# Performance work log

Measured on AMD Instinct MI355X. Metric: run time of the kernel, lower is better.

The kernel has to match this reference:

```python
import jax, jax.numpy as jnp
import numpy as np

GAMMA = 1.0
BIG = 1e10  # finite stand-in for +inf boundary; exp(-BIG) underflows to exactly 0 (grad-safe)


def setup_inputs() -> dict:
    key = jax.random.key(0)
    k1, k2 = jax.random.split(key)
    B, L, C = 64, 1024, 64
    x = jax.random.normal(k1, (B, L, C), dtype=jnp.float32)
    y = jax.random.normal(k2, (B, L, C), dtype=jnp.float32)
    return {"x": x, "y": y}


def _soft_dtw(x, y, gamma=GAMMA):
    B, L, C = x.shape
    # squared-euclidean pairwise cost, scaled by 1/gamma (matches torch code)
    x2 = jnp.sum(x * x, axis=-1)[:, :, None]            # [B,L,1]
    y2 = jnp.sum(y * y, axis=-1)[:, None, :]            # [B,1,L]
    D = (x2 + y2 - 2.0 * jnp.einsum('blc,bmc->blm', x, y)) / gamma  # [B,L,L]

    # Anti-diagonal wavefront DP over the (L+2)x(L+2) R matrix.
    # r_d[i] holds R[i, d-i] for the diagonal i+j=d, i in 0..L+1.
    n = L + 2
    ii = jnp.arange(n)
    i_idx = jnp.clip(ii - 1, 0, L - 1)
    r_prev2 = jnp.full((B, n), BIG, dtype=x.dtype).at[:, 0].set(0.0)  # diag d=0: R[0,0]=0
    r_prev1 = jnp.full((B, n), BIG, dtype=x.dtype)                    # diag d=1: all boundary
    big_col = jnp.full((B, 1), BIG, dtype=x.dtype)

    def step(carry, d):
        rp2, rp1 = carry
        jj = d - ii
        valid = (ii >= 1) & (ii <= L) & (jj >= 1) & (jj <= L)
        j_idx = jnp.clip(jj - 1, 0, L - 1)
        d_vals = D[:, i_idx, j_idx]                                   # [B,n] cost along diagonal
        r_diag = jnp.concatenate([big_col, rp2[:, :-1]], axis=1)      # R[i-1, j-1]
        r_up   = jnp.concatenate([big_col, rp1[:, :-1]], axis=1)      # R[i-1, j]
        r_left = rp1                                                  # R[i,   j-1]
        z = jnp.stack([-r_diag, -r_up, -r_left], axis=-1)             # [B,n,3]
        zmax = jnp.max(z, axis=-1)
        softmin = -(jnp.log(jnp.sum(jnp.exp(z - zmax[..., None]), axis=-1)) + zmax)
        new = jnp.where(valid[None, :], d_vals + softmin, BIG)
        return (rp1, new), None

    (_, r_last), _ = jax.lax.scan(step, (r_prev2, r_prev1), jnp.arange(2, 2 * L + 1))
    # last diagonal is d=2L; R[L,L] sits at index i=L
    return r_last[:, L] * gamma


def reference(x, y):
    return _soft_dtw(x, y)
```

## Files before the change

kernel.cpp:

```cpp
#include <hip/hip_runtime.h>


typedef unsigned short ushort_t;
typedef __attribute__((ext_vector_type(8))) short short8;
typedef __attribute__((ext_vector_type(4))) float f32x4;
typedef __attribute__((ext_vector_type(4))) unsigned short ushort4v;

constexpr int B_ = 64, L_ = 1024, C_ = 64;
constexpr int DSTR = 130;
constexpr int HBSTR = 1280;

#define BIGV 1e10f
#define INV_LN2 1.44269504088896340736f
#define LN2F 0.69314718055994530942f
#define DPP_WAVE_SHL1 0x130
#define DPP_WAVE_SHR1 0x138

static __device__ __forceinline__ ushort_t f2bf(float f) {
  unsigned u = __builtin_bit_cast(unsigned, f);
  unsigned r = (u + 0x7fffu + ((u >> 16) & 1u)) >> 16;
  return (ushort_t)r;
}
static __device__ __forceinline__ float exp2_(float x) {
  float r; asm("v_exp_f32 %0, %1" : "=v"(r) : "v"(x)); return r;
}
static __device__ __forceinline__ float log2_(float x) {
  float r; asm("v_log_f32 %0, %1" : "=v"(r) : "v"(x)); return r;
}
static __device__ __forceinline__ unsigned cvt_pk_bf16(float lo, float hi) {
  unsigned r; asm("v_cvt_pk_bf16_f32 %0, %1, %2" : "=v"(r) : "v"(lo), "v"(hi)); return r;
}
static __device__ __forceinline__ float dpp_shr1(float old, float src) {
  return __builtin_bit_cast(float, __builtin_amdgcn_update_dpp(
      __builtin_bit_cast(int, old), __builtin_bit_cast(int, src),
      DPP_WAVE_SHR1, 0xF, 0xF, false));
}
static __device__ __forceinline__ float dpp_shl1(float v) {
  return __builtin_bit_cast(float, __builtin_amdgcn_update_dpp(
      __builtin_bit_cast(int, v), __builtin_bit_cast(int, v),
      DPP_WAVE_SHL1, 0xF, 0xF, false));
}

__global__ __launch_bounds__(256) void prep_kernel(
    const float* __restrict__ x, const float* __restrict__ y,
    ushort_t* __restrict__ xb, ushort_t* __restrict__ yb,
    float* __restrict__ x2, float* __restrict__ y2, int* __restrict__ flagsG)
{
  if (blockIdx.x == 0 && threadIdx.x < 192) flagsG[threadIdx.x] = 0;
  const int lane = threadIdx.x & 63;
  const int sub = lane >> 4;
  const int cg  = lane & 15;
  const int wv = (blockIdx.x * blockDim.x + threadIdx.x) >> 6;
  const int nw = (gridDim.x * blockDim.x) >> 6;
  const int totalGroups = (2 * B_ * L_) >> 2;
  for (int g = wv; g < totalGroups; g += nw) {
    int r = g * 4 + sub;
    const float* src; ushort_t* dst; float* nrm;
    if (r < B_ * L_) { src = x; dst = xb; nrm = x2; }
    else             { r -= B_ * L_; src = y; dst = yb; nrm = y2; }
    const float4 v = *(const float4*)(src + (size_t)r * C_ + cg * 4);
    ushort4v p;
    p.x = f2bf(v.x); p.y = f2bf(v.y); p.z = f2bf(v.z); p.w = f2bf(v.w);
    *(ushort4v*)(dst + (size_t)r * C_ + cg * 4) = p;
    float s = v.x*v.x + v.y*v.y + v.z*v.z + v.w*v.w;
    s += __shfl_xor(s, 1); s += __shfl_xor(s, 2);
    s += __shfl_xor(s, 4); s += __shfl_xor(s, 8);
    if (cg == 0) nrm[r] = s * INV_LN2;
  }
}

template<int HDST, bool FIRST>
static __device__ __forceinline__ void dp_chunk(
    const int t, const int lane, float& cur, float& dgp, float hvv,
    const float zsel, const ushort_t* __restrict__ DtwLane,
    float* __restrict__ HbDst, float* __restrict__ HXB)
{
  const unsigned* pw = (const unsigned*)(DtwLane + ((t << 6) & 127));
  const int cb = (t << 6) - 63;
  unsigned a0 = pw[0], a1 = pw[1], b0 = pw[2], b1 = pw[3];

  auto step = [&](unsigned dw, int k, int u) -> float {
    float dv = __builtin_bit_cast(float, (k & 1) ? (dw & 0xffff0000u) : (dw << 16));
    float up = dpp_shr1(hvv, cur);
    float dg = dgp, lf = cur;
    if constexpr (FIRST) {
      bool at0 = (u == lane);
      dg = at0 ? zsel : dg;
      lf = at0 ? BIGV : lf;
    }
    float mn = fminf(fminf(up, dg), lf);
    float e = exp2_(mn - up) + exp2_(mn - dg) + exp2_(mn - lf);
    float nv = (dv + mn) - log2_(e);
    dgp = up;
    hvv = dpp_shl1(hvv);
    if constexpr (FIRST) { if (u >= lane) cur = nv; }
    else cur = nv;
    return nv;
  };
  auto flush4 = [&](int c0, float v0, float v1, float v2, float v3) {
    if constexpr (HDST == 0) {
      if (lane == 63) { HbDst[c0] = v0; HbDst[c0+1] = v1; HbDst[c0+2] = v2; HbDst[c0+3] = v3; }
    } else if constexpr (HDST == 1) {
      if (lane == 63) { HXB[c0] = v0; HXB[c0+1] = v1; HXB[c0+2] = v2; HXB[c0+3] = v3; }
    }
  };

  #pragma unroll 1
  for (int g = 0; g < 8; ++g) {
    const int u0 = g * 8;
    unsigned n0 = 0, n1 = 0, n2 = 0, n3 = 0;
    if (g < 7) {
      n0 = pw[u0/2 + 4]; n1 = pw[u0/2 + 5]; n2 = pw[u0/2 + 6]; n3 = pw[u0/2 + 7];
    }
    float v0 = step(a0, 0, u0 + 0);
    float v1 = step(a0, 1, u0 + 1);
    float v2 = step(a1, 0, u0 + 2);
    float v3 = step(a1, 1, u0 + 3);
    if constexpr (!FIRST) flush4(cb + u0, v0, v1, v2, v3);
    float v4 = step(b0, 0, u0 + 4);
    float v5 = step(b0, 1, u0 + 5);
    float v6 = step(b1, 0, u0 + 6);
    float v7 = step(b1, 1, u0 + 7);
    if constexpr (!FIRST) flush4(cb + u0 + 4, v4, v5, v6, v7);
    a0 = n0; a1 = n1; b0 = n2; b1 = n3;
    (void)v0; (void)v1; (void)v2; (void)v3; (void)v4; (void)v5; (void)v6; (void)v7;
  }
  if constexpr (FIRST) {
    if constexpr (HDST == 0) { if (lane == 63) HbDst[0] = cur; }
    else if constexpr (HDST == 1) { if (lane == 63) HXB[0] = cur; }
  }
}

template<int HDST>
static __device__ __forceinline__ void dp_tail(
    const int lane, float& cur, float& dgp,
    const ushort_t* __restrict__ DtwLane,
    float* __restrict__ HbDst, float* __restrict__ HXB)
{
  const unsigned* pw = (const unsigned*)(DtwLane);
  #pragma unroll 1
  for (int g = 0; g < 8; ++g) {
    unsigned w0 = pw[g*4], w1 = pw[g*4+1], w2 = pw[g*4+2], w3 = pw[g*4+3];
    #pragma unroll
    for (int k = 0; k < 8; ++k) {
      const int u = g * 8 + k;
      unsigned dw = (k < 2) ? w0 : (k < 4) ? w1 : (k < 6) ? w2 : w3;
      float dv = __builtin_bit_cast(float, (k & 1) ? (dw & 0xffff0000u) : (dw << 16));
      float up = dpp_shr1(BIGV, cur);
      float dg = dgp, lf = cur;
      float mn = fminf(fminf(up, dg), lf);
      float e = exp2_(mn - up) + exp2_(mn - dg) + exp2_(mn - lf);
      float nv = (dv + mn) - log2_(e);
      dgp = up;
      if (u < lane) {
        cur = nv;
        if constexpr (HDST == 0) { if (lane == 63) HbDst[961 + u] = nv; }
        else if constexpr (HDST == 1) { if (lane == 63) HXB[961 + u] = nv; }
      }
    }
  }
}

static __device__ __forceinline__ void spin_lds(int* f, int v) {
  int k = 0;
  while (__hip_atomic_load(f, __ATOMIC_ACQUIRE, __HIP_MEMORY_SCOPE_WORKGROUP) < v) {
    __builtin_amdgcn_s_sleep(1);
    if (++k > (1 << 26)) break;
  }
}
static __device__ __forceinline__ void spin_glb(int* f, int v) {
  int k = 0;
  while (__hip_atomic_load(f, __ATOMIC_ACQUIRE, __HIP_MEMORY_SCOPE_AGENT) < v) {
    __builtin_amdgcn_s_sleep(8);
    if (++k > (1 << 26)) break;
  }
}

template<int HSRC, int HDST>
static __device__ __forceinline__ void run_band(
    const ushort_t* __restrict__ xbB, const ushort_t* __restrict__ ybB,
    const float* __restrict__ x2B, const float* __restrict__ y2B,
    const float* __restrict__ HXin, float* __restrict__ HXout,
    int* __restrict__ fGin, int* __restrict__ fGout,
    ushort_t* __restrict__ Dtw, const float* __restrict__ HbSrc,
    float* __restrict__ HbDst, int* __restrict__ cin, int* __restrict__ cout,
    const int lane, const int W, float* __restrict__ outp)
{
  const int m = lane & 15, q = lane >> 4;
  const int i0 = W * 64;

  short8 af[4][2];
  #pragma unroll
  for (int mt = 0; mt < 4; ++mt)
    #pragma unroll
    for (int ks = 0; ks < 2; ++ks)
      af[mt][ks] = *(const short8*)(xbB + (size_t)(i0 + mt * 16 + m) * C_ + ks * 32 + q * 8);
  f32x4 x2q[4];
  #pragma unroll
  for (int mt = 0; mt < 4; ++mt) x2q[mt] = *(const f32x4*)(x2B + i0 + mt * 16 + q * 4);

  short8 bfr0[4], bfr1[4];
  auto load_bfr = [&](int tc) {
    const ushort_t* yb0 = ybB + (size_t)tc * 64 * C_;
    #pragma unroll
    for (int nt = 0; nt < 4; ++nt) {
      bfr0[nt] = *(const short8*)(yb0 + (size_t)(nt * 16 + m) * C_ + q * 8);
      bfr1[nt] = *(const short8*)(yb0 + (size_t)(nt * 16 + m) * C_ + 32 + q * 8);
    }
  };
  auto gram = [&](int tc) {
    const int cb = tc * 64;
    const float* y2j = y2B + cb;
    #pragma unroll
    for (int mt = 0; mt < 4; ++mt) {
      const int r0 = mt * 16 + q * 4;
      #pragma unroll
      for (int nt = 0; nt < 4; ++nt) {
        f32x4 acc = {0.f, 0.f, 0.f, 0.f};
        acc = __builtin_amdgcn_mfma_f32_16x16x32_bf16(af[mt][0], bfr0[nt], acc, 0, 0, 0);
        acc = __builtin_amdgcn_mfma_f32_16x16x32_bf16(af[mt][1], bfr1[nt], acc, 0, 0, 0);
        float y2v = y2j[nt * 16 + m];
        float d0 = fmaf(acc[0], -2.f * INV_LN2, x2q[mt][0] + y2v);
        float d1 = fmaf(acc[1], -2.f * INV_LN2, x2q[mt][1] + y2v);
        float d2 = fmaf(acc[2], -2.f * INV_LN2, x2q[mt][2] + y2v);
        float d3 = fmaf(acc[3], -2.f * INV_LN2, x2q[mt][3] + y2v);
        unsigned p01 = cvt_pk_bf16(d0, d1);
        unsigned p23 = cvt_pk_bf16(d2, d3);
        const int cs = cb + nt * 16 + m + r0;
        ushort_t* base = Dtw + r0 * DSTR;
        base[             ( cs      & 127)] = (ushort_t)p01;
        base[    DSTR  +  ((cs + 1) & 127)] = (ushort_t)(p01 >> 16);
        base[2 * DSTR  +  ((cs + 2) & 127)] = (ushort_t)p23;
        base[3 * DSTR  +  ((cs + 3) & 127)] = (ushort_t)(p23 >> 16);
      }
    }
  };

  float cur = 0.f, dgp = BIGV;
  const float zsel = (W == 0 && lane == 0) ? 0.f : BIGV;
  const ushort_t* DtwLane = Dtw + lane * DSTR;

  load_bfr(0);
  gram(0);

  #pragma unroll 1
  for (int t = 0; t < 16; ++t) {
    if (t < 15) load_bfr(t + 1);
    float hvv;
    if constexpr (HSRC == 0) {
      hvv = BIGV;
    } else if constexpr (HSRC == 1) {
      spin_lds(cin, t + 1);
      hvv = HbSrc[(t << 6) + lane];
    } else {
      spin_glb(fGin, t + 1);
      hvv = HXin[(t << 6) + lane];
    }
    if (t == 0) dp_chunk<HDST, true >(0, lane, cur, dgp, hvv, zsel, DtwLane, HbDst, HXout);
    else        dp_chunk<HDST, false>(t, lane, cur, dgp, hvv, zsel, DtwLane, HbDst, HXout);
    if constexpr (HDST == 0) {
      if (lane == 0) __hip_atomic_store(cout, t, __ATOMIC_RELEASE, __HIP_MEMORY_SCOPE_WORKGROUP);
    } else if constexpr (HDST == 1) {
      if (lane == 0) __hip_atomic_store(fGout, t, __ATOMIC_RELEASE, __HIP_MEMORY_SCOPE_AGENT);
    }
    if (t < 15) gram(t + 1);
  }
  dp_tail<HDST>(lane, cur, dgp, DtwLane, HbDst, HXout);
  if constexpr (HDST == 0) {
    if (lane == 0) __hip_atomic_store(cout, 16, __ATOMIC_RELEASE, __HIP_MEMORY_SCOPE_WORKGROUP);
  } else if constexpr (HDST == 1) {
    if (lane == 0) __hip_atomic_store(fGout, 16, __ATOMIC_RELEASE, __HIP_MEMORY_SCOPE_AGENT);
  }
  if (W == 15 && lane == 63) *outp = cur * LN2F;
}

__global__ __launch_bounds__(256) void sdtw_kernel(
    const ushort_t* __restrict__ xb, const ushort_t* __restrict__ yb,
    const float* __restrict__ x2g, const float* __restrict__ y2g,
    float* __restrict__ HXg, int* __restrict__ flagsG,
    float* __restrict__ out)
{
  __shared__ ushort_t Dt[4][64 * DSTR];
  __shared__ float Hb[3][HBSTR];
  __shared__ int cflag[4];

  const int b = blockIdx.x & 63;
  const int sub = blockIdx.x >> 6;
  const int w = threadIdx.x >> 6;
  const int lane = threadIdx.x & 63;
  const int W = sub * 4 + w;

  if (threadIdx.x < 4) cflag[threadIdx.x] = 0;
  __syncthreads();

  const ushort_t* xbB = xb + (size_t)b * L_ * C_;
  const ushort_t* ybB = yb + (size_t)b * L_ * C_;
  const float* x2B = x2g + b * L_;
  const float* y2B = y2g + b * L_;
  const float* HXin = HXg + ((size_t)b * 3 + (sub - 1)) * L_;
  float* HXout      = HXg + ((size_t)b * 3 + sub) * L_;
  int* fGin  = flagsG + b * 3 + (sub - 1);
  int* fGout = flagsG + b * 3 + sub;
  ushort_t* Dtw = &Dt[w][0];
  const float* HbSrc = (w > 0) ? &Hb[w - 1][0] : &Hb[0][0];
  float* HbDst = (w < 3) ? &Hb[w][0] : &Hb[0][0];
  int* cin  = (w > 0) ? &cflag[w - 1] : &cflag[0];
  int* cout = (w < 3) ? &cflag[w] : &cflag[3];
  float* outp = out + b;

  if (sub == 0) {
    if (w == 0)      run_band<0, 0>(xbB, ybB, x2B, y2B, HXin, HXout, fGin, fGout, Dtw, HbSrc, HbDst, cin, cout, lane, W, outp);
    else if (w < 3)  run_band<1, 0>(xbB, ybB, x2B, y2B, HXin, HXout, fGin, fGout, Dtw, HbSrc, HbDst, cin, cout, lane, W, outp);
    else             run_band<1, 1>(xbB, ybB, x2B, y2B, HXin, HXout, fGin, fGout, Dtw, HbSrc, HbDst, cin, cout, lane, W, outp);
  } else if (sub < 3) {
    if (w == 0)      run_band<2, 0>(xbB, ybB, x2B, y2B, HXin, HXout, fGin, fGout, Dtw, HbSrc, HbDst, cin, cout, lane, W, outp);
    else if (w < 3)  run_band<1, 0>(xbB, ybB, x2B, y2B, HXin, HXout, fGin, fGout, Dtw, HbSrc, HbDst, cin, cout, lane, W, outp);
    else             run_band<1, 1>(xbB, ybB, x2B, y2B, HXin, HXout, fGin, fGout, Dtw, HbSrc, HbDst, cin, cout, lane, W, outp);
  } else {
    if (w == 0)      run_band<2, 0>(xbB, ybB, x2B, y2B, HXin, HXout, fGin, fGout, Dtw, HbSrc, HbDst, cin, cout, lane, W, outp);
    else if (w < 3)  run_band<1, 0>(xbB, ybB, x2B, y2B, HXin, HXout, fGin, fGout, Dtw, HbSrc, HbDst, cin, cout, lane, W, outp);
    else             run_band<1, 2>(xbB, ybB, x2B, y2B, HXin, HXout, fGin, fGout, Dtw, HbSrc, HbDst, cin, cout, lane, W, outp);
  }
}

extern "C" void kernel_launch(void* const* d_in, const int* in_sizes, int n_in,
                              void* d_out, int out_size, void* d_ws, size_t ws_size,
                              hipStream_t stream) {
  const float* x = (const float*)d_in[0];
  const float* y = (const float*)d_in[1];
  float* out = (float*)d_out;

  char* ws = (char*)d_ws;
  const size_t XB = (size_t)B_ * L_ * C_ * 2;
  const size_t NB = (size_t)B_ * L_ * 4;
  ushort_t* xb = (ushort_t*)ws;
  ushort_t* yb = (ushort_t*)(ws + XB);
  float* x2 = (float*)(ws + 2 * XB);
  float* y2 = (float*)(ws + 2 * XB + NB);
  float* HX = (float*)(ws + 2 * XB + 2 * NB);
  int* flagsG = (int*)(ws + 2 * XB + 2 * NB + (size_t)B_ * 3 * L_ * 4);

  prep_kernel<<<512, 256, 0, stream>>>(x, y, xb, yb, x2, y2, flagsG);
  sdtw_kernel<<<256, 256, 0, stream>>>(xb, yb, x2, y2, HX, flagsG, out);
}
```

Before: 355.3 us.

## Replace log-sum-exp DP with scaled linear-domain recurrence using mantissa/exponent pairs

The soft-min recurrence moves out of log space. Each R cell is stored as a mantissa plus an integer base-2 exponent, so a step needs three ldexp scalings, a sum and a multiply by a precomputed exp2 of the fractional cost, instead of three exps and a log. The gram stage now precomputes, per cell, the integer part of the cost and an fp16 exp2 of its fractional part, packed into 32-bit LDS words. Halo buffers double in size to carry (mantissa, exponent) pairs, and the global spin sleep is shortened. The fp16 cost factor and integer flooring change numerics relative to the fp32 log-space reference.

```diff
diff --git a/kernel.cpp b/kernel.cpp
--- a/kernel.cpp
+++ b/kernel.cpp
@@ -7,38 +7,33 @@
 typedef __attribute__((ext_vector_type(4))) unsigned short ushort4v;
 
 constexpr int B_ = 64, L_ = 1024, C_ = 64;
-constexpr int DSTR = 130;
-constexpr int HBSTR = 1280;
-
-#define BIGV 1e10f
+constexpr int DSTRW = 129;
+
+#define BIGS (-(1 << 24))
 #define INV_LN2 1.44269504088896340736f
 #define LN2F 0.69314718055994530942f
-#define DPP_WAVE_SHL1 0x130
-#define DPP_WAVE_SHR1 0x138
 
 static __device__ __forceinline__ ushort_t f2bf(float f) {
   unsigned u = __builtin_bit_cast(unsigned, f);
   unsigned r = (u + 0x7fffu + ((u >> 16) & 1u)) >> 16;
   return (ushort_t)r;
 }
-static __device__ __forceinline__ float exp2_(float x) {
-  float r; asm("v_exp_f32 %0, %1" : "=v"(r) : "v"(x)); return r;
-}
-static __device__ __forceinline__ float log2_(float x) {
-  float r; asm("v_log_f32 %0, %1" : "=v"(r) : "v"(x)); return r;
-}
-static __device__ __forceinline__ unsigned cvt_pk_bf16(float lo, float hi) {
-  unsigned r; asm("v_cvt_pk_bf16_f32 %0, %1, %2" : "=v"(r) : "v"(lo), "v"(hi)); return r;
-}
 static __device__ __forceinline__ float dpp_shr1(float old, float src) {
   return __builtin_bit_cast(float, __builtin_amdgcn_update_dpp(
-      __builtin_bit_cast(int, old), __builtin_bit_cast(int, src),
-      DPP_WAVE_SHR1, 0xF, 0xF, false));
+      __builtin_bit_cast(int, old), __builtin_bit_cast(int, src), 0x138, 0xF, 0xF, false));
+}
+static __device__ __forceinline__ int dpp_shr1_i(int old, int src) {
+  return __builtin_amdgcn_update_dpp(old, src, 0x138, 0xF, 0xF, false);
 }
 static __device__ __forceinline__ float dpp_shl1(float v) {
   return __builtin_bit_cast(float, __builtin_amdgcn_update_dpp(
-      __builtin_bit_cast(int, v), __builtin_bit_cast(int, v),
-      DPP_WAVE_SHL1, 0xF, 0xF, false));
+      __builtin_bit_cast(int, v), __builtin_bit_cast(int, v), 0x130, 0xF, 0xF, false));
+}
+static __device__ __forceinline__ int dpp_shl1_i(int v) {
+  return __builtin_amdgcn_update_dpp(v, v, 0x130, 0xF, 0xF, false);
+}
+static __device__ __forceinline__ int imax3(int a, int b, int c) {
+  int m = a > b ? a : b; return c > m ? c : m;
 }
 
 __global__ __launch_bounds__(256) void prep_kernel(
@@ -65,97 +60,113 @@
     float s = v.x*v.x + v.y*v.y + v.z*v.z + v.w*v.w;
     s += __shfl_xor(s, 1); s += __shfl_xor(s, 2);
     s += __shfl_xor(s, 4); s += __shfl_xor(s, 8);
-    if (cg == 0) nrm[r] = s * INV_LN2;
+    if (cg == 0) nrm[r] = s * INV_LN2 + 0.25f;
   }
 }
 
 template<int HDST, bool FIRST>
 static __device__ __forceinline__ void dp_chunk(
-    const int t, const int lane, float& cur, float& dgp, float hvv,
-    const float zsel, const ushort_t* __restrict__ DtwLane,
-    float* __restrict__ HbDst, float* __restrict__ HXB)
-{
-  const unsigned* pw = (const unsigned*)(DtwLane + ((t << 6) & 127));
+    const int t, const int lane,
+    float& cur_u, int& cur_S, float& dgp_u, int& dgp_S,
+    float hv_u, int hv_S, const float zu, const int zS,
+    const unsigned* __restrict__ DtLane,
+    float2* __restrict__ HbDst, float2* __restrict__ HXB)
+{
+  const unsigned* pw = DtLane + ((t & 1) << 6);
   const int cb = (t << 6) - 63;
-  unsigned a0 = pw[0], a1 = pw[1], b0 = pw[2], b1 = pw[3];
-
-  auto step = [&](unsigned dw, int k, int u) -> float {
-    float dv = __builtin_bit_cast(float, (k & 1) ? (dw & 0xffff0000u) : (dw << 16));
-    float up = dpp_shr1(hvv, cur);
-    float dg = dgp, lf = cur;
+  unsigned d0=pw[0],d1=pw[1],d2=pw[2],d3=pw[3],d4=pw[4],d5=pw[5],d6=pw[6],d7=pw[7];
+
+  auto step = [&](unsigned dw, int u) {
+    float up_u = dpp_shr1(hv_u, cur_u);
+    int   up_S = dpp_shr1_i(hv_S, cur_S);
+    hv_u = dpp_shl1(hv_u);
+    hv_S = dpp_shl1_i(hv_S);
+    float p = (float)__builtin_bit_cast(_Float16, (unsigned short)(dw & 0xffffu));
+    int di = (int)(dw >> 16);
+    float dg_u = dgp_u, lf_u = cur_u;
+    int   dg_S = dgp_S, lf_S = cur_S;
     if constexpr (FIRST) {
-      bool at0 = (u == lane);
-      dg = at0 ? zsel : dg;
-      lf = at0 ? BIGV : lf;
-    }
-    float mn = fminf(fminf(up, dg), lf);
-    float e = exp2_(mn - up) + exp2_(mn - dg) + exp2_(mn - lf);
-    float nv = (dv + mn) - log2_(e);
-    dgp = up;
-    hvv = dpp_shl1(hvv);
-    if constexpr (FIRST) { if (u >= lane) cur = nv; }
-    else cur = nv;
-    return nv;
-  };
-  auto flush4 = [&](int c0, float v0, float v1, float v2, float v3) {
-    if constexpr (HDST == 0) {
-      if (lane == 63) { HbDst[c0] = v0; HbDst[c0+1] = v1; HbDst[c0+2] = v2; HbDst[c0+3] = v3; }
-    } else if constexpr (HDST == 1) {
-      if (lane == 63) { HXB[c0] = v0; HXB[c0+1] = v1; HXB[c0+2] = v2; HXB[c0+3] = v3; }
+      const bool a0 = (u == lane);
+      dg_u = a0 ? zu : dg_u;  dg_S = a0 ? zS : dg_S;
+      lf_u = a0 ? 0.f : lf_u; lf_S = a0 ? BIGS : lf_S;
+    }
+    int Sm = imax3(up_S, dg_S, lf_S);
+    float sa = ldexpf(up_u, up_S - Sm);
+    float sb = ldexpf(dg_u, dg_S - Sm);
+    float sc = ldexpf(lf_u, lf_S - Sm);
+    float un = ((sa + sb) + sc) * p;
+    int ub = __float_as_int(un);
+    int ex = ((ub >> 23) & 0xff) - 126;
+    float mant = __int_as_float((ub & 0x007fffff) | 0x3f000000);
+    int Sn = Sm - di + ex;
+    dgp_u = up_u; dgp_S = up_S;
+    const bool wr = FIRST ? (u >= lane) : true;
+    if (wr) { cur_u = mant; cur_S = Sn; }
+    if constexpr (!FIRST && HDST != 2) {
+      if (lane == 63) {
+        float2 pr; pr.x = mant; pr.y = __int_as_float(Sn);
+        if constexpr (HDST == 0) HbDst[cb + u] = pr;
+        else                     HXB[cb + u] = pr;
+      }
     }
   };
 
   #pragma unroll 1
   for (int g = 0; g < 8; ++g) {
-    const int u0 = g * 8;
-    unsigned n0 = 0, n1 = 0, n2 = 0, n3 = 0;
+    unsigned n0=0,n1=0,n2=0,n3=0,n4=0,n5=0,n6=0,n7=0;
     if (g < 7) {
-      n0 = pw[u0/2 + 4]; n1 = pw[u0/2 + 5]; n2 = pw[u0/2 + 6]; n3 = pw[u0/2 + 7];
-    }
-    float v0 = step(a0, 0, u0 + 0);
-    float v1 = step(a0, 1, u0 + 1);
-    float v2 = step(a1, 0, u0 + 2);
-    float v3 = step(a1, 1, u0 + 3);
-    if constexpr (!FIRST) flush4(cb + u0, v0, v1, v2, v3);
-    float v4 = step(b0, 0, u0 + 4);
-    float v5 = step(b0, 1, u0 + 5);
-    float v6 = step(b1, 0, u0 + 6);
-    float v7 = step(b1, 1, u0 + 7);
-    if constexpr (!FIRST) flush4(cb + u0 + 4, v4, v5, v6, v7);
-    a0 = n0; a1 = n1; b0 = n2; b1 = n3;
-    (void)v0; (void)v1; (void)v2; (void)v3; (void)v4; (void)v5; (void)v6; (void)v7;
-  }
-  if constexpr (FIRST) {
-    if constexpr (HDST == 0) { if (lane == 63) HbDst[0] = cur; }
-    else if constexpr (HDST == 1) { if (lane == 63) HXB[0] = cur; }
+      const unsigned* np = pw + ((g + 1) << 3);
+      n0=np[0]; n1=np[1]; n2=np[2]; n3=np[3]; n4=np[4]; n5=np[5]; n6=np[6]; n7=np[7];
+    }
+    const int u0 = g << 3;
+    step(d0, u0+0); step(d1, u0+1); step(d2, u0+2); step(d3, u0+3);
+    step(d4, u0+4); step(d5, u0+5); step(d6, u0+6); step(d7, u0+7);
+    d0=n0; d1=n1; d2=n2; d3=n3; d4=n4; d5=n5; d6=n6; d7=n7;
+  }
+  if constexpr (FIRST && HDST != 2) {
+    if (lane == 63) {
+      float2 pr; pr.x = cur_u; pr.y = __int_as_float(cur_S);
+      if constexpr (HDST == 0) HbDst[0] = pr; else HXB[0] = pr;
+    }
   }
 }
 
 template<int HDST>
 static __device__ __forceinline__ void dp_tail(
-    const int lane, float& cur, float& dgp,
-    const ushort_t* __restrict__ DtwLane,
-    float* __restrict__ HbDst, float* __restrict__ HXB)
-{
-  const unsigned* pw = (const unsigned*)(DtwLane);
+    const int lane, float& cur_u, int& cur_S, float& dgp_u, int& dgp_S,
+    const unsigned* __restrict__ DtLane,
+    float2* __restrict__ HbDst, float2* __restrict__ HXB)
+{
+  const unsigned* pw = DtLane;
   #pragma unroll 1
   for (int g = 0; g < 8; ++g) {
-    unsigned w0 = pw[g*4], w1 = pw[g*4+1], w2 = pw[g*4+2], w3 = pw[g*4+3];
+    unsigned w0=pw[g*8],w1=pw[g*8+1],w2=pw[g*8+2],w3=pw[g*8+3],
+             w4=pw[g*8+4],w5=pw[g*8+5],w6=pw[g*8+6],w7=pw[g*8+7];
     #pragma unroll
     for (int k = 0; k < 8; ++k) {
       const int u = g * 8 + k;
-      unsigned dw = (k < 2) ? w0 : (k < 4) ? w1 : (k < 6) ? w2 : w3;
-      float dv = __builtin_bit_cast(float, (k & 1) ? (dw & 0xffff0000u) : (dw << 16));
-      float up = dpp_shr1(BIGV, cur);
-      float dg = dgp, lf = cur;
-      float mn = fminf(fminf(up, dg), lf);
-      float e = exp2_(mn - up) + exp2_(mn - dg) + exp2_(mn - lf);
-      float nv = (dv + mn) - log2_(e);
-      dgp = up;
+      unsigned dw = (k==0)?w0:(k==1)?w1:(k==2)?w2:(k==3)?w3:(k==4)?w4:(k==5)?w5:(k==6)?w6:w7;
+      float up_u = dpp_shr1(0.f, cur_u);
+      int   up_S = dpp_shr1_i(BIGS, cur_S);
+      float p = (float)__builtin_bit_cast(_Float16, (unsigned short)(dw & 0xffffu));
+      int di = (int)(dw >> 16);
+      int Sm = imax3(up_S, dgp_S, cur_S);
+      float sa = ldexpf(up_u, up_S - Sm);
+      float sb = ldexpf(dgp_u, dgp_S - Sm);
+      float sc = ldexpf(cur_u, cur_S - Sm);
+      float un = ((sa + sb) + sc) * p;
+      int ub = __float_as_int(un);
+      int ex = ((ub >> 23) & 0xff) - 126;
+      float mant = __int_as_float((ub & 0x007fffff) | 0x3f000000);
+      int Sn = Sm - di + ex;
+      dgp_u = up_u; dgp_S = up_S;
       if (u < lane) {
-        cur = nv;
-        if constexpr (HDST == 0) { if (lane == 63) HbDst[961 + u] = nv; }
-        else if constexpr (HDST == 1) { if (lane == 63) HXB[961 + u] = nv; }
+        cur_u = mant; cur_S = Sn;
+        if (lane == 63) {
+          float2 pr; pr.x = mant; pr.y = __int_as_float(Sn);
+          if constexpr (HDST == 0) HbDst[961 + u] = pr;
+          else if constexpr (HDST == 1) HXB[961 + u] = pr;
+        }
       }
     }
   }
@@ -171,7 +182,7 @@
 static __device__ __forceinline__ void spin_glb(int* f, int v) {
   int k = 0;
   while (__hip_atomic_load(f, __ATOMIC_ACQUIRE, __HIP_MEMORY_SCOPE_AGENT) < v) {
-    __builtin_amdgcn_s_sleep(8);
+    __builtin_amdgcn_s_sleep(2);
     if (++k > (1 << 26)) break;
   }
 }
@@ -180,10 +191,10 @@
 static __device__ __forceinline__ void run_band(
     const ushort_t* __restrict__ xbB, const ushort_t* __restrict__ ybB,
     const float* __restrict__ x2B, const float* __restrict__ y2B,
-    const float* __restrict__ HXin, float* __restrict__ HXout,
+    const float2* __restrict__ HXin, float2* __restrict__ HXout,
     int* __restrict__ fGin, int* __restrict__ fGout,
-    ushort_t* __restrict__ Dtw, const float* __restrict__ HbSrc,
-    float* __restrict__ HbDst, int* __restrict__ cin, int* __restrict__ cout,
+    unsigned* __restrict__ Dtw, const float2* __restrict__ HbSrc,
+    float2* __restrict__ HbDst, int* __restrict__ cin, int* __restrict__ cout,
     const int lane, const int W, float* __restrict__ outp)
 {
   const int m = lane & 15, q = lane >> 4;
@@ -200,17 +211,18 @@
   for (int mt = 0; mt < 4; ++mt) x2q[mt] = *(const f32x4*)(x2B + i0 + mt * 16 + q * 4);
 
   short8 bfr0[4], bfr1[4];
+  f32x4 y2r = {0.f, 0.f, 0.f, 0.f};
   auto load_bfr = [&](int tc) {
     const ushort_t* yb0 = ybB + (size_t)tc * 64 * C_;
     #pragma unroll
     for (int nt = 0; nt < 4; ++nt) {
       bfr0[nt] = *(const short8*)(yb0 + (size_t)(nt * 16 + m) * C_ + q * 8);
       bfr1[nt] = *(const short8*)(yb0 + (size_t)(nt * 16 + m) * C_ + 32 + q * 8);
+      y2r[nt] = y2B[tc * 64 + nt * 16 + m];
     }
   };
   auto gram = [&](int tc) {
     const int cb = tc * 64;
-    const float* y2j = y2B + cb;
     #pragma unroll
     for (int mt = 0; mt < 4; ++mt) {
       const int r0 = mt * 16 + q * 4;
@@ -219,26 +231,34 @@
         f32x4 acc = {0.f, 0.f, 0.f, 0.f};
         acc = __builtin_amdgcn_mfma_f32_16x16x32_bf16(af[mt][0], bfr0[nt], acc, 0, 0, 0);
         acc = __builtin_amdgcn_mfma_f32_16x16x32_bf16(af[mt][1], bfr1[nt], acc, 0, 0, 0);
-        float y2v = y2j[nt * 16 + m];
-        float d0 = fmaf(acc[0], -2.f * INV_LN2, x2q[mt][0] + y2v);
-        float d1 = fmaf(acc[1], -2.f * INV_LN2, x2q[mt][1] + y2v);
-        float d2 = fmaf(acc[2], -2.f * INV_LN2, x2q[mt][2] + y2v);
-        float d3 = fmaf(acc[3], -2.f * INV_LN2, x2q[mt][3] + y2v);
-        unsigned p01 = cvt_pk_bf16(d0, d1);
-        unsigned p23 = cvt_pk_bf16(d2, d3);
+        const float y2v = y2r[nt];
         const int cs = cb + nt * 16 + m + r0;
-        ushort_t* base = Dtw + r0 * DSTR;
-        base[             ( cs      & 127)] = (ushort_t)p01;
-        base[    DSTR  +  ((cs + 1) & 127)] = (ushort_t)(p01 >> 16);
-        base[2 * DSTR  +  ((cs + 2) & 127)] = (ushort_t)p23;
-        base[3 * DSTR  +  ((cs + 3) & 127)] = (ushort_t)(p23 >> 16);
+        #pragma unroll
+        for (int reg = 0; reg < 4; ++reg) {
+          float d = fmaf(acc[reg], -2.f * INV_LN2, x2q[mt][reg] + y2v);
+          d = fmaxf(d, 0.5f);
+          int di = (int)d;
+          float pe = (float)di + 0.5f - d;
+          float p = __builtin_amdgcn_exp2f(pe);
+          unsigned short hb = __builtin_bit_cast(unsigned short, (_Float16)p);
+          Dtw[(r0 + reg) * DSTRW + ((cs + reg) & 127)] = ((unsigned)di << 16) | (unsigned)hb;
+        }
       }
     }
   };
-
-  float cur = 0.f, dgp = BIGV;
-  const float zsel = (W == 0 && lane == 0) ? 0.f : BIGV;
-  const ushort_t* DtwLane = Dtw + lane * DSTR;
+  auto signal = [&](int v) {
+    if constexpr (HDST == 0) {
+      if (lane == 0) __hip_atomic_store(cout, v, __ATOMIC_RELEASE, __HIP_MEMORY_SCOPE_WORKGROUP);
+    } else if constexpr (HDST == 1) {
+      if (lane == 0) __hip_atomic_store(fGout, v, __ATOMIC_RELEASE, __HIP_MEMORY_SCOPE_AGENT);
+    }
+  };
+
+  float cur_u = 0.f, dgp_u = 0.f;
+  int cur_S = BIGS, dgp_S = BIGS;
+  const float zu = (W == 0 && lane == 0) ? 1.0f : 0.f;
+  const int   zS = (W == 0 && lane == 0) ? 0 : BIGS;
+  const unsigned* DtLane = Dtw + lane * DSTRW;
 
   load_bfr(0);
   gram(0);
@@ -246,42 +266,41 @@
   #pragma unroll 1
   for (int t = 0; t < 16; ++t) {
     if (t < 15) load_bfr(t + 1);
-    float hvv;
+    float hv_u; int hv_S;
     if constexpr (HSRC == 0) {
-      hvv = BIGV;
+      hv_u = 0.f; hv_S = BIGS;
     } else if constexpr (HSRC == 1) {
       spin_lds(cin, t + 1);
-      hvv = HbSrc[(t << 6) + lane];
+      float2 pr = HbSrc[(t << 6) + lane];
+      hv_u = pr.x; hv_S = __float_as_int(pr.y);
     } else {
       spin_glb(fGin, t + 1);
-      hvv = HXin[(t << 6) + lane];
-    }
-    if (t == 0) dp_chunk<HDST, true >(0, lane, cur, dgp, hvv, zsel, DtwLane, HbDst, HXout);
-    else        dp_chunk<HDST, false>(t, lane, cur, dgp, hvv, zsel, DtwLane, HbDst, HXout);
-    if constexpr (HDST == 0) {
-      if (lane == 0) __hip_atomic_store(cout, t, __ATOMIC_RELEASE, __HIP_MEMORY_SCOPE_WORKGROUP);
-    } else if constexpr (HDST == 1) {
-      if (lane == 0) __hip_atomic_store(fGout, t, __ATOMIC_RELEASE, __HIP_MEMORY_SCOPE_AGENT);
-    }
+      float2 pr = HXin[(t << 6) + lane];
+      hv_u = pr.x; hv_S = __float_as_int(pr.y);
+    }
+    if (t == 0)
+      dp_chunk<HDST, true >(0, lane, cur_u, cur_S, dgp_u, dgp_S, hv_u, hv_S, zu, zS, DtLane, HbDst, HXout);
+    else
+      dp_chunk<HDST, false>(t, lane, cur_u, cur_S, dgp_u, dgp_S, hv_u, hv_S, zu, zS, DtLane, HbDst, HXout);
+    signal(t);
     if (t < 15) gram(t + 1);
   }
-  dp_tail<HDST>(lane, cur, dgp, DtwLane, HbDst, HXout);
-  if constexpr (HDST == 0) {
-    if (lane == 0) __hip_atomic_store(cout, 16, __ATOMIC_RELEASE, __HIP_MEMORY_SCOPE_WORKGROUP);
-  } else if constexpr (HDST == 1) {
-    if (lane == 0) __hip_atomic_store(fGout, 16, __ATOMIC_RELEASE, __HIP_MEMORY_SCOPE_AGENT);
-  }
-  if (W == 15 && lane == 63) *outp = cur * LN2F;
+  dp_tail<HDST>(lane, cur_u, cur_S, dgp_u, dgp_S, DtLane, HbDst, HXout);
+  signal(16);
+  if (W == 15 && lane == 63) {
+    float uu = fmaxf(cur_u, 1e-30f);
+    *outp = (-(float)cur_S - __builtin_amdgcn_logf(uu)) * LN2F;
+  }
 }
 
 __global__ __launch_bounds__(256) void sdtw_kernel(
     const ushort_t* __restrict__ xb, const ushort_t* __restrict__ yb,
     const float* __restrict__ x2g, const float* __restrict__ y2g,
-    float* __restrict__ HXg, int* __restrict__ flagsG,
+    float2* __restrict__ HXg, int* __restrict__ flagsG,
     float* __restrict__ out)
 {
-  __shared__ ushort_t Dt[4][64 * DSTR];
-  __shared__ float Hb[3][HBSTR];
+  __shared__ unsigned Dt[4][64 * DSTRW];
+  __shared__ float2 Hb[3][1024];
   __shared__ int cflag[4];
 
   const int b = blockIdx.x & 63;
@@ -297,13 +316,13 @@
   const ushort_t* ybB = yb + (size_t)b * L_ * C_;
   const float* x2B = x2g + b * L_;
   const float* y2B = y2g + b * L_;
-  const float* HXin = HXg + ((size_t)b * 3 + (sub - 1)) * L_;
-  float* HXout      = HXg + ((size_t)b * 3 + sub) * L_;
-  int* fGin  = flagsG + b * 3 + (sub - 1);
-  int* fGout = flagsG + b * 3 + sub;
-  ushort_t* Dtw = &Dt[w][0];
-  const float* HbSrc = (w > 0) ? &Hb[w - 1][0] : &Hb[0][0];
-  float* HbDst = (w < 3) ? &Hb[w][0] : &Hb[0][0];
+  const float2* HXin = HXg + ((size_t)b * 3 + (sub > 0 ? sub - 1 : 0)) * L_;
+  float2* HXout      = HXg + ((size_t)b * 3 + (sub < 3 ? sub : 2)) * L_;
+  int* fGin  = flagsG + b * 3 + (sub > 0 ? sub - 1 : 0);
+  int* fGout = flagsG + b * 3 + (sub < 3 ? sub : 2);
+  unsigned* Dtw = &Dt[w][0];
+  const float2* HbSrc = (w > 0) ? &Hb[w - 1][0] : &Hb[0][0];
+  float2* HbDst = (w < 3) ? &Hb[w][0] : &Hb[0][0];
   int* cin  = (w > 0) ? &cflag[w - 1] : &cflag[0];
   int* cout = (w < 3) ? &cflag[w] : &cflag[3];
   float* outp = out + b;
@@ -337,8 +356,8 @@
   ushort_t* yb = (ushort_t*)(ws + XB);
   float* x2 = (float*)(ws + 2 * XB);
   float* y2 = (float*)(ws + 2 * XB + NB);
-  float* HX = (float*)(ws + 2 * XB + 2 * NB);
-  int* flagsG = (int*)(ws + 2 * XB + 2 * NB + (size_t)B_ * 3 * L_ * 4);
+  float2* HX = (float2*)(ws + 2 * XB + 2 * NB);
+  int* flagsG = (int*)(ws + 2 * XB + 2 * NB + (size_t)B_ * 3 * L_ * 8);
 
   prep_kernel<<<512, 256, 0, stream>>>(x, y, xb, yb, x2, y2, flagsG);
   sdtw_kernel<<<256, 256, 0, stream>>>(xb, yb, x2, y2, HX, flagsG, out);
```

After: 469.5 us. +32.1%, slower.

## Use 8-wave blocks with two blocks per batch and a cheaper softmin

Applied to the files above, without the earlier changes.

Each batch element is now handled by 2 blocks of 8 waves (512 threads) instead of 4 blocks of 4 waves. That replaces two of the three cross-block global-flag handoffs with in-LDS handoffs between waves. The softmin is rewritten to sort the three inputs so that one exp2 becomes the constant 1, leaving two exp2 plus a log. The global spin sleep is also shortened. The larger block needs more LDS and registers per workgroup, which may limit residency.

```diff
diff --git a/kernel.cpp b/kernel.cpp
--- a/kernel.cpp
+++ b/kernel.cpp
@@ -8,37 +8,26 @@
 
 constexpr int B_ = 64, L_ = 1024, C_ = 64;
 constexpr int DSTR = 130;
-constexpr int HBSTR = 1280;
 
 #define BIGV 1e10f
 #define INV_LN2 1.44269504088896340736f
 #define LN2F 0.69314718055994530942f
-#define DPP_WAVE_SHL1 0x130
-#define DPP_WAVE_SHR1 0x138
 
 static __device__ __forceinline__ ushort_t f2bf(float f) {
   unsigned u = __builtin_bit_cast(unsigned, f);
   unsigned r = (u + 0x7fffu + ((u >> 16) & 1u)) >> 16;
   return (ushort_t)r;
 }
-static __device__ __forceinline__ float exp2_(float x) {
-  float r; asm("v_exp_f32 %0, %1" : "=v"(r) : "v"(x)); return r;
-}
-static __device__ __forceinline__ float log2_(float x) {
-  float r; asm("v_log_f32 %0, %1" : "=v"(r) : "v"(x)); return r;
-}
 static __device__ __forceinline__ unsigned cvt_pk_bf16(float lo, float hi) {
   unsigned r; asm("v_cvt_pk_bf16_f32 %0, %1, %2" : "=v"(r) : "v"(lo), "v"(hi)); return r;
 }
 static __device__ __forceinline__ float dpp_shr1(float old, float src) {
   return __builtin_bit_cast(float, __builtin_amdgcn_update_dpp(
-      __builtin_bit_cast(int, old), __builtin_bit_cast(int, src),
-      DPP_WAVE_SHR1, 0xF, 0xF, false));
+      __builtin_bit_cast(int, old), __builtin_bit_cast(int, src), 0x138, 0xF, 0xF, false));
 }
 static __device__ __forceinline__ float dpp_shl1(float v) {
   return __builtin_bit_cast(float, __builtin_amdgcn_update_dpp(
-      __builtin_bit_cast(int, v), __builtin_bit_cast(int, v),
-      DPP_WAVE_SHL1, 0xF, 0xF, false));
+      __builtin_bit_cast(int, v), __builtin_bit_cast(int, v), 0x130, 0xF, 0xF, false));
 }
 
 __global__ __launch_bounds__(256) void prep_kernel(
@@ -46,7 +35,7 @@
     ushort_t* __restrict__ xb, ushort_t* __restrict__ yb,
     float* __restrict__ x2, float* __restrict__ y2, int* __restrict__ flagsG)
 {
-  if (blockIdx.x == 0 && threadIdx.x < 192) flagsG[threadIdx.x] = 0;
+  if (blockIdx.x == 0 && threadIdx.x < 64) flagsG[threadIdx.x] = 0;
   const int lane = threadIdx.x & 63;
   const int sub = lane >> 4;
   const int cg  = lane & 15;
@@ -72,10 +61,10 @@
 template<int HDST, bool FIRST>
 static __device__ __forceinline__ void dp_chunk(
     const int t, const int lane, float& cur, float& dgp, float hvv,
-    const float zsel, const ushort_t* __restrict__ DtwLane,
+    const float zsel, const ushort_t* __restrict__ DtLane,
     float* __restrict__ HbDst, float* __restrict__ HXB)
 {
-  const unsigned* pw = (const unsigned*)(DtwLane + ((t << 6) & 127));
+  const unsigned* pw = (const unsigned*)(DtLane + ((t << 6) & 127));
   const int cb = (t << 6) - 63;
   unsigned a0 = pw[0], a1 = pw[1], b0 = pw[2], b1 = pw[3];
 
@@ -89,8 +78,10 @@
       lf = at0 ? BIGV : lf;
     }
     float mn = fminf(fminf(up, dg), lf);
-    float e = exp2_(mn - up) + exp2_(mn - dg) + exp2_(mn - lf);
-    float nv = (dv + mn) - log2_(e);
+    float mx = fmaxf(fmaxf(up, dg), lf);
+    float md = fmaxf(fminf(up, dg), fminf(fmaxf(up, dg), lf));
+    float e = 1.0f + (__builtin_amdgcn_exp2f(mn - md) + __builtin_amdgcn_exp2f(mn - mx));
+    float nv = (dv + mn) - __builtin_amdgcn_logf(e);
     dgp = up;
     hvv = dpp_shl1(hvv);
     if constexpr (FIRST) { if (u >= lane) cur = nv; }
@@ -134,10 +125,10 @@
 template<int HDST>
 static __device__ __forceinline__ void dp_tail(
     const int lane, float& cur, float& dgp,
-    const ushort_t* __restrict__ DtwLane,
+    const ushort_t* __restrict__ DtLane,
     float* __restrict__ HbDst, float* __restrict__ HXB)
 {
-  const unsigned* pw = (const unsigned*)(DtwLane);
+  const unsigned* pw = (const unsigned*)(DtLane);
   #pragma unroll 1
   for (int g = 0; g < 8; ++g) {
     unsigned w0 = pw[g*4], w1 = pw[g*4+1], w2 = pw[g*4+2], w3 = pw[g*4+3];
@@ -149,13 +140,17 @@
       float up = dpp_shr1(BIGV, cur);
       float dg = dgp, lf = cur;
       float mn = fminf(fminf(up, dg), lf);
-      float e = exp2_(mn - up) + exp2_(mn - dg) + exp2_(mn - lf);
-      float nv = (dv + mn) - log2_(e);
+      float mx = fmaxf(fmaxf(up, dg), lf);
+      float md = fmaxf(fminf(up, dg), fminf(fmaxf(up, dg), lf));
+      float e = 1.0f + (__builtin_amdgcn_exp2f(mn - md) + __builtin_amdgcn_exp2f(mn - mx));
+      float nv = (dv + mn) - __builtin_amdgcn_logf(e);
       dgp = up;
       if (u < lane) {
         cur = nv;
-        if constexpr (HDST == 0) { if (lane == 63) HbDst[961 + u] = nv; }
-        else if constexpr (HDST == 1) { if (lane == 63) HXB[961 + u] = nv; }
+        if (lane == 63) {
+          if constexpr (HDST == 0) HbDst[961 + u] = nv;
+          else if constexpr (HDST == 1) HXB[961 + u] = nv;
+        }
       }
     }
   }
@@ -171,7 +166,7 @@
 static __device__ __forceinline__ void spin_glb(int* f, int v) {
   int k = 0;
   while (__hip_atomic_load(f, __ATOMIC_ACQUIRE, __HIP_MEMORY_SCOPE_AGENT) < v) {
-    __builtin_amdgcn_s_sleep(8);
+    __builtin_amdgcn_s_sleep(2);
     if (++k > (1 << 26)) break;
   }
 }
@@ -235,10 +230,17 @@
       }
     }
   };
+  auto signal = [&](int v) {
+    if constexpr (HDST == 0) {
+      if (lane == 0) __hip_atomic_store(cout, v, __ATOMIC_RELEASE, __HIP_MEMORY_SCOPE_WORKGROUP);
+    } else if constexpr (HDST == 1) {
+      if (lane == 0) __hip_atomic_store(fGout, v, __ATOMIC_RELEASE, __HIP_MEMORY_SCOPE_AGENT);
+    }
+  };
 
   float cur = 0.f, dgp = BIGV;
-  const float zsel = (W == 0 && lane == 0) ? 0.f : BIGV;
-  const ushort_t* DtwLane = Dtw + lane * DSTR;
+  const float zsel = (W == 0 && lane == 0) ? 0.0f : BIGV;
+  const ushort_t* DtLane = Dtw + lane * DSTR;
 
   load_bfr(0);
   gram(0);
@@ -256,70 +258,64 @@
       spin_glb(fGin, t + 1);
       hvv = HXin[(t << 6) + lane];
     }
-    if (t == 0) dp_chunk<HDST, true >(0, lane, cur, dgp, hvv, zsel, DtwLane, HbDst, HXout);
-    else        dp_chunk<HDST, false>(t, lane, cur, dgp, hvv, zsel, DtwLane, HbDst, HXout);
-    if constexpr (HDST == 0) {
-      if (lane == 0) __hip_atomic_store(cout, t, __ATOMIC_RELEASE, __HIP_MEMORY_SCOPE_WORKGROUP);
-    } else if constexpr (HDST == 1) {
-      if (lane == 0) __hip_atomic_store(fGout, t, __ATOMIC_RELEASE, __HIP_MEMORY_SCOPE_AGENT);
-    }
+    if (t == 0) dp_chunk<HDST, true >(0, lane, cur, dgp, hvv, zsel, DtLane, HbDst, HXout);
+    else        dp_chunk<HDST, false>(t, lane, cur, dgp, hvv, zsel, DtLane, HbDst, HXout);
+    signal(t);
     if (t < 15) gram(t + 1);
   }
-  dp_tail<HDST>(lane, cur, dgp, DtwLane, HbDst, HXout);
-  if constexpr (HDST == 0) {
-    if (lane == 0) __hip_atomic_store(cout, 16, __ATOMIC_RELEASE, __HIP_MEMORY_SCOPE_WORKGROUP);
-  } else if constexpr (HDST == 1) {
-    if (lane == 0) __hip_atomic_store(fGout, 16, __ATOMIC_RELEASE, __HIP_MEMORY_SCOPE_AGENT);
-  }
+  dp_tail<HDST>(lane, cur, dgp, DtLane, HbDst, HXout);
+  signal(16);
   if (W == 15 && lane == 63) *outp = cur * LN2F;
 }
 
-__global__ __launch_bounds__(256) void sdtw_kernel(
+__global__ __launch_bounds__(512) void sdtw_kernel(
     const ushort_t* __restrict__ xb, const ushort_t* __restrict__ yb,
     const float* __restrict__ x2g, const float* __restrict__ y2g,
     float* __restrict__ HXg, int* __restrict__ flagsG,
     float* __restrict__ out)
 {
-  __shared__ ushort_t Dt[4][64 * DSTR];
-  __shared__ float Hb[3][HBSTR];
-  __shared__ int cflag[4];
+  __shared__ ushort_t Dt[8][64 * DSTR];
+  __shared__ float Hb[7][1024];
+  __shared__ int cflag[8];
 
   const int b = blockIdx.x & 63;
   const int sub = blockIdx.x >> 6;
   const int w = threadIdx.x >> 6;
   const int lane = threadIdx.x & 63;
-  const int W = sub * 4 + w;
-
-  if (threadIdx.x < 4) cflag[threadIdx.x] = 0;
+  const int W = sub * 8 + w;
+
+  if (threadIdx.x < 8) cflag[threadIdx.x] = 0;
   __syncthreads();
 
   const ushort_t* xbB = xb + (size_t)b * L_ * C_;
   const ushort_t* ybB = yb + (size_t)b * L_ * C_;
   const float* x2B = x2g + b * L_;
   const float* y2B = y2g + b * L_;
-  const float* HXin = HXg + ((size_t)b * 3 + (sub - 1)) * L_;
-  float* HXout      = HXg + ((size_t)b * 3 + sub) * L_;
-  int* fGin  = flagsG + b * 3 + (sub - 1);
-  int* fGout = flagsG + b * 3 + sub;
+  const float* HXin = HXg + (size_t)b * L_;
+  float* HXout     = HXg + (size_t)b * L_;
+  int* fGin  = flagsG + b;
+  int* fGout = flagsG + b;
   ushort_t* Dtw = &Dt[w][0];
   const float* HbSrc = (w > 0) ? &Hb[w - 1][0] : &Hb[0][0];
-  float* HbDst = (w < 3) ? &Hb[w][0] : &Hb[0][0];
+  float* HbDst = (w < 7) ? &Hb[w][0] : &Hb[0][0];
   int* cin  = (w > 0) ? &cflag[w - 1] : &cflag[0];
-  int* cout = (w < 3) ? &cflag[w] : &cflag[3];
+  int* cout = (w < 7) ? &cflag[w] : &cflag[7];
   float* outp = out + b;
 
   if (sub == 0) {
-    if (w == 0)      run_band<0, 0>(xbB, ybB, x2B, y2B, HXin, HXout, fGin, fGout, Dtw, HbSrc, HbDst, cin, cout, lane, W, outp);
-    else if (w < 3)  run_band<1, 0>(xbB, ybB, x2B, y2B, HXin, HXout, fGin, fGout, Dtw, HbSrc, HbDst, cin, cout, lane, W, outp);
-    else             run_band<1, 1>(xbB, ybB, x2B, y2B, HXin, HXout, fGin, fGout, Dtw, HbSrc, HbDst, cin, cout, lane, W, outp);
-  } else if (sub < 3) {
-    if (w == 0)      run_band<2, 0>(xbB, ybB, x2B, y2B, HXin, HXout, fGin, fGout, Dtw, HbSrc, HbDst, cin, cout, lane, W, outp);
-    else if (w < 3)  run_band<1, 0>(xbB, ybB, x2B, y2B, HXin, HXout, fGin, fGout, Dtw, HbSrc, HbDst, cin, cout, lane, W, outp);
-    else             run_band<1, 1>(xbB, ybB, x2B, y2B, HXin, HXout, fGin, fGout, Dtw, HbSrc, HbDst, cin, cout, lane, W, outp);
+    if (w == 0)
+      run_band<0, 0>(xbB, ybB, x2B, y2B, HXin, HXout, fGin, fGout, Dtw, HbSrc, HbDst, cin, cout, lane, W, outp);
+    else if (w < 7)
+      run_band<1, 0>(xbB, ybB, x2B, y2B, HXin, HXout, fGin, fGout, Dtw, HbSrc, HbDst, cin, cout, lane, W, outp);
+    else
+      run_band<1, 1>(xbB, ybB, x2B, y2B, HXin, HXout, fGin, fGout, Dtw, HbSrc, HbDst, cin, cout, lane, W, outp);
   } else {
-    if (w == 0)      run_band<2, 0>(xbB, ybB, x2B, y2B, HXin, HXout, fGin, fGout, Dtw, HbSrc, HbDst, cin, cout, lane, W, outp);
-    else if (w < 3)  run_band<1, 0>(xbB, ybB, x2B, y2B, HXin, HXout, fGin, fGout, Dtw, HbSrc, HbDst, cin, cout, lane, W, outp);
-    else             run_band<1, 2>(xbB, ybB, x2B, y2B, HXin, HXout, fGin, fGout, Dtw, HbSrc, HbDst, cin, cout, lane, W, outp);
+    if (w == 0)
+      run_band<2, 0>(xbB, ybB, x2B, y2B, HXin, HXout, fGin, fGout, Dtw, HbSrc, HbDst, cin, cout, lane, W, outp);
+    else if (w < 7)
+      run_band<1, 0>(xbB, ybB, x2B, y2B, HXin, HXout, fGin, fGout, Dtw, HbSrc, HbDst, cin, cout, lane, W, outp);
+    else
+      run_band<1, 2>(xbB, ybB, x2B, y2B, HXin, HXout, fGin, fGout, Dtw, HbSrc, HbDst, cin, cout, lane, W, outp);
   }
 }
 
@@ -338,8 +334,8 @@
   float* x2 = (float*)(ws + 2 * XB);
   float* y2 = (float*)(ws + 2 * XB + NB);
   float* HX = (float*)(ws + 2 * XB + 2 * NB);
-  int* flagsG = (int*)(ws + 2 * XB + 2 * NB + (size_t)B_ * 3 * L_ * 4);
+  int* flagsG = (int*)(ws + 2 * XB + 3 * NB);
 
   prep_kernel<<<512, 256, 0, stream>>>(x, y, xb, yb, x2, y2, flagsG);
-  sdtw_kernel<<<256, 256, 0, stream>>>(xb, yb, x2, y2, HX, flagsG, out);
-}
+  sdtw_kernel<<<128, 512, 0, stream>>>(xb, yb, x2, y2, HX, flagsG, out);
+}
```

After: 383.6 us. 1.08x slower.
